# Kernel tuning notes

Hardware: AMD Instinct MI355X
Metric: run time of the kernel (lower is better)

The kernel has to match this reference:

```python
import jax, jax.numpy as jnp
import numpy as np

NUM_HEADS = 16


def setup_inputs() -> dict:
    key = jax.random.key(0)
    k1, k2, k3 = jax.random.split(key, 3)
    x = jax.random.normal(k1, (2, 2048, 1024), dtype=jnp.float32)
    w_qkv = jax.random.normal(k2, (3072, 1024), dtype=jnp.float32) * 0.02
    b_qkv = jax.random.normal(k3, (3072,), dtype=jnp.float32) * 0.02
    return {"x": x, "w_qkv": w_qkv, "b_qkv": b_qkv}


def reference(x, w_qkv, b_qkv):
    b, s, _ = x.shape
    d_model = w_qkv.shape[0] // 3
    head_dim = d_model // NUM_HEADS
    # fused QKV projection (torch Linear: x @ W^T + b)
    qkv = x @ w_qkv.T + b_qkv                      # [b, s, 3*d_model]
    qkv = qkv.reshape(b, s, NUM_HEADS, 3 * head_dim)
    qkv = jnp.transpose(qkv, (0, 2, 1, 3))          # [b, h, s, 3*hd]
    q, k, v = jnp.split(qkv, 3, axis=-1)            # each [b, h, s, hd]
    scale = 1.0 / np.sqrt(head_dim).astype(np.float32)
    scores = jnp.einsum("bhqd,bhkd->bhqk", q, k) * scale
    attn = jax.nn.softmax(scores, axis=-1)
    values = jnp.einsum("bhqk,bhkd->bhqd", attn, v)  # [b, h, s, hd]
    # Faithful to source: reshape WITHOUT permuting heads back (head-interleaved)
    return values.reshape(b, s, d_model)
```

## Files before the change

kernel.cpp:

```cpp
#include <hip/hip_runtime.h>
#include <cstdint>

typedef unsigned short ushort_t;

#define M_ROWS 4096
#define N_COLS 3072
#define K_DIM  1024
#define S_LEN  2048
#define NHEADS 16
#define HDIM   64
#define QSCALE 0.1803368801111204f

typedef __bf16 bf16_t;
typedef bf16_t  bf16x8  __attribute__((ext_vector_type(8)));
typedef short   shortx4 __attribute__((ext_vector_type(4)));
typedef float   floatx4 __attribute__((ext_vector_type(4)));
typedef ushort_t ushortx4 __attribute__((ext_vector_type(4)));

union U32x2S4 { unsigned u[2]; shortx4 s; };

__device__ __forceinline__ unsigned short f2bf(float f) {
  unsigned u = __float_as_uint(f);
  u += 0x7FFFu + ((u >> 16) & 1u);
  return (unsigned short)(u >> 16);
}

__device__ __forceinline__ unsigned pkbf(float a, float b) {
  unsigned ua = __float_as_uint(a) + 0x8000u;
  unsigned ub = __float_as_uint(b) + 0x8000u;
  return __builtin_amdgcn_perm(ub, ua, 0x07060302u);
}

__device__ __forceinline__ unsigned cvtpk(float a, float b) {
#if __has_builtin(__builtin_amdgcn_cvt_pk_bf16_f32)
  auto t = __builtin_amdgcn_cvt_pk_bf16_f32(a, b);
  unsigned r;
  __builtin_memcpy(&r, &t, 4);
  return r;
#else
  return pkbf(a, b);
#endif
}

__device__ __forceinline__ float fexp2(float x) {
#if __has_builtin(__builtin_amdgcn_exp2f)
  return __builtin_amdgcn_exp2f(x);
#else
  float r; asm volatile("v_exp_f32 %0, %1\n\ts_nop 1" : "=v"(r) : "v"(x)); return r;
#endif
}

__device__ __forceinline__ void gload_lds16(const void* g, void* l) {
  __builtin_amdgcn_global_load_lds(
      (const __attribute__((address_space(1))) unsigned int*)g,
      (__attribute__((address_space(3))) unsigned int*)l,
      16, 0, 0);
}

__global__ __launch_bounds__(256) void cvt_bf16_kernel(
    const float* __restrict__ x, const float* __restrict__ w,
    ushort_t* __restrict__ Xb, ushort_t* __restrict__ Wb) {
  const int NX8 = (M_ROWS * K_DIM) / 8;
  int i = blockIdx.x * 256 + threadIdx.x;
  const float4* src;
  ushort_t* dst;
  int idx;
  if (i < NX8) { src = (const float4*)x; dst = Xb; idx = i; }
  else         { src = (const float4*)w; dst = Wb; idx = i - NX8; }
  float4 a = src[2 * idx];
  float4 b = src[2 * idx + 1];
  uint4 o;
  o.x = cvtpk(a.x, a.y);
  o.y = cvtpk(a.z, a.w);
  o.z = cvtpk(b.x, b.y);
  o.w = cvtpk(b.z, b.w);
  *(uint4*)(dst + 8 * (size_t)idx) = o;
}

__global__ __launch_bounds__(256) void qkv_gemm_kernel(
    const ushort_t* __restrict__ Xb, const ushort_t* __restrict__ Wb,
    const float* __restrict__ bias,
    ushort_t* __restrict__ Qb, ushort_t* __restrict__ Kb, ushort_t* __restrict__ Vb) {
  __shared__ ushort_t As[128 * 64];
  __shared__ ushort_t Bs[128 * 64];
  const int tid = threadIdx.x;
  const int l = tid & 63, w = tid >> 6;
  const int quad = l >> 4, lj = l & 15;
  const int m0 = blockIdx.y * 128, n0 = blockIdx.x * 128;
  const int wm = (w & 1) * 64, wn = (w >> 1) * 64;

  floatx4 acc[4][4] = {};

  const int srow = w * 32 + (l >> 3);
  const int scol = ((l & 7) ^ (l >> 3)) * 8;
  const ushort_t* gA = Xb + (size_t)(m0 + srow) * K_DIM + scol;
  const ushort_t* gB = Wb + (size_t)(n0 + srow) * K_DIM + scol;
  ushort_t* lA = As + (w * 32) * 64;
  ushort_t* lB = Bs + (w * 32) * 64;

  const int swr = lj & 7;

  for (int k0 = 0; k0 < K_DIM; k0 += 64) {
    __syncthreads();
#pragma unroll
    for (int c = 0; c < 4; ++c) {
      gload_lds16(gA + (size_t)(c * 8) * K_DIM + k0, lA + c * 8 * 64);
      gload_lds16(gB + (size_t)(c * 8) * K_DIM + k0, lB + c * 8 * 64);
    }
    __syncthreads();
#pragma unroll
    for (int kk = 0; kk < 2; ++kk) {
      const int ch = ((kk * 4 + quad) ^ swr) * 8;
      bf16x8 aF[4], bF[4];
#pragma unroll
      for (int i = 0; i < 4; ++i)
        aF[i] = *(const bf16x8*)(As + (wm + i * 16 + lj) * 64 + ch);
#pragma unroll
      for (int j = 0; j < 4; ++j)
        bF[j] = *(const bf16x8*)(Bs + (wn + j * 16 + lj) * 64 + ch);
#pragma unroll
      for (int i = 0; i < 4; ++i)
#pragma unroll
        for (int j = 0; j < 4; ++j)
          acc[i][j] = __builtin_amdgcn_mfma_f32_16x16x32_bf16(aF[i], bF[j], acc[i][j], 0, 0, 0);
    }
  }

#pragma unroll
  for (int j = 0; j < 4; ++j) {
    const int n = n0 + wn + j * 16 + lj;
    const int h = n / 192;
    const int r = n - h * 192;
    const int seg = r >> 6;
    const int d = r & 63;
    const float bv = bias[n];
    ushort_t* dst = (seg == 0) ? Qb : (seg == 1) ? Kb : Vb;
    const float scl = (seg == 0) ? QSCALE : 1.0f;
    const size_t base = (size_t)h * S_LEN * HDIM + d;
#pragma unroll
    for (int i = 0; i < 4; ++i) {
#pragma unroll
      for (int rg = 0; rg < 4; ++rg) {
        const int m = m0 + wm + i * 16 + quad * 4 + rg;
        const int bi = m >> 11;
        const int si = m & 2047;
        dst[base + ((size_t)bi * NHEADS * S_LEN + si) * HDIM] =
            f2bf((acc[i][j][rg] + bv) * scl);
      }
    }
  }
}

__global__ __launch_bounds__(512, 2) void attn_kernel(
    const ushort_t* __restrict__ Qb, const ushort_t* __restrict__ Kb,
    const ushort_t* __restrict__ Vb, float* __restrict__ out) {
  __shared__ ushort_t Ks[2][128 * 64];
  __shared__ ushort_t Vs[2][64 * 140];
  const int tid = threadIdx.x;
  const int l = tid & 63, w = tid >> 6;
  const int quad = l >> 4, lj = l & 15;
  const int id = (blockIdx.x & 7) * 32 + (blockIdx.x >> 3);
  const int bh = id >> 3;
  const int qt = id & 7;
  const int q0 = qt * 256 + w * 32;
  const size_t headoff = (size_t)bh * S_LEN * HDIM;

  bf16x8 qF[2][2];
#pragma unroll
  for (int qh = 0; qh < 2; ++qh)
#pragma unroll
    for (int kk = 0; kk < 2; ++kk)
      qF[qh][kk] = *(const bf16x8*)(Qb + headoff +
                                    (size_t)(q0 + qh * 16 + lj) * HDIM +
                                    kk * 32 + quad * 8);

  floatx4 accO[2][4] = {};
  float l_runA[2] = {0.f, 0.f}, l_runB[2] = {0.f, 0.f};

  const int kr = tid >> 3;
  const int kc = ((tid & 7) ^ (kr & 7)) * 8;
  const ushort_t* gK = Kb + headoff + (size_t)kr * HDIM + kc;

  const int dq = tid & 15;
  const int spw = tid >> 4;
  const ushort_t* gV = Vb + headoff + dq * 4;
  const int swz = (dq >> 2) << 1;

  const int swk = lj & 7;

  {
    uint2 va[2], vb[2];
#pragma unroll
    for (int R = 0; R < 2; ++R) {
      const ushort_t* g = gV + (size_t)(2 * (R * 32 + spw)) * HDIM;
      va[R] = *(const uint2*)g;
      vb[R] = *(const uint2*)(g + HDIM);
    }
#pragma unroll
    for (int c = 0; c < 2; ++c)
      gload_lds16(gK + (size_t)(c * 64) * HDIM, &Ks[0][0] + tid * 8 + c * 64 * 64);
    unsigned* vdst = (unsigned*)&Vs[0][0];
#pragma unroll
    for (int R = 0; R < 2; ++R) {
      const int sp = R * 32 + spw;
      unsigned o0 = __builtin_amdgcn_perm(vb[R].x, va[R].x, 0x05040100u);
      unsigned o1 = __builtin_amdgcn_perm(vb[R].x, va[R].x, 0x07060302u);
      unsigned o2 = __builtin_amdgcn_perm(vb[R].y, va[R].y, 0x05040100u);
      unsigned o3 = __builtin_amdgcn_perm(vb[R].y, va[R].y, 0x07060302u);
      const int sp2 = sp ^ swz;
      vdst[(4 * dq + 0) * 70 + sp2] = o0;
      vdst[(4 * dq + 1) * 70 + sp2] = o1;
      vdst[(4 * dq + 2) * 70 + sp2] = o2;
      vdst[(4 * dq + 3) * 70 + sp2] = o3;
    }
  }
  __syncthreads();

  for (int kb = 0; kb < 16; ++kb) {
    const int cur = kb & 1;
    const ushort_t* Kc = &Ks[cur][0];
    const ushort_t* Vc = &Vs[cur][0];

    uint2 va[2], vb[2];
    if (kb < 15) {
      const int kv1 = (kb + 1) * 128;
#pragma unroll
      for (int R = 0; R < 2; ++R) {
        const ushort_t* g = gV + (size_t)(kv1 + 2 * (R * 32 + spw)) * HDIM;
        va[R] = *(const uint2*)g;
        vb[R] = *(const uint2*)(g + HDIM);
      }
#pragma unroll
      for (int c = 0; c < 2; ++c)
        gload_lds16(gK + (size_t)(kv1 + c * 64) * HDIM,
                    &Ks[cur ^ 1][0] + tid * 8 + c * 64 * 64);
    }

    floatx4 accST[2][8];
#pragma unroll
    for (int c = 0; c < 8; ++c) {
      const ushort_t* krow = Kc + (c * 16 + lj) * 64;
      bf16x8 kF0 = *(const bf16x8*)(krow + ((quad ^ swk) * 8));
      bf16x8 kF1 = *(const bf16x8*)(krow + (((quad ^ swk) ^ 4) * 8));
#pragma unroll
      for (int qh = 0; qh < 2; ++qh) {
        floatx4 z = {0.f, 0.f, 0.f, 0.f};
        z = __builtin_amdgcn_mfma_f32_16x16x32_bf16(kF0, qF[qh][0], z, 0, 0, 0);
        accST[qh][c] =
            __builtin_amdgcn_mfma_f32_16x16x32_bf16(kF1, qF[qh][1], z, 0, 0, 0);
      }
    }

    shortx4 aP[2][8];
#pragma unroll
    for (int qh = 0; qh < 2; ++qh) {
      float lsA = 0.f, lsB = 0.f;
#pragma unroll
      for (int c = 0; c < 8; ++c) {
        float p0 = fexp2(accST[qh][c][0]);
        float p1 = fexp2(accST[qh][c][1]);
        float p2 = fexp2(accST[qh][c][2]);
        float p3 = fexp2(accST[qh][c][3]);
        lsA += p0 + p1;
        lsB += p2 + p3;
        U32x2S4 t;
        t.u[0] = cvtpk(p0, p1);
        t.u[1] = cvtpk(p2, p3);
        aP[qh][c] = t.s;
      }
      l_runA[qh] += lsA;
      l_runB[qh] += lsB;
    }

    if (kb < 15) {
      unsigned* vdst = (unsigned*)&Vs[cur ^ 1][0];
#pragma unroll
      for (int R = 0; R < 2; ++R) {
        const int sp = R * 32 + spw;
        unsigned o0 = __builtin_amdgcn_perm(vb[R].x, va[R].x, 0x05040100u);
        unsigned o1 = __builtin_amdgcn_perm(vb[R].x, va[R].x, 0x07060302u);
        unsigned o2 = __builtin_amdgcn_perm(vb[R].y, va[R].y, 0x05040100u);
        unsigned o3 = __builtin_amdgcn_perm(vb[R].y, va[R].y, 0x07060302u);
        const int sp2 = sp ^ swz;
        vdst[(4 * dq + 0) * 70 + sp2] = o0;
        vdst[(4 * dq + 1) * 70 + sp2] = o1;
        vdst[(4 * dq + 2) * 70 + sp2] = o2;
        vdst[(4 * dq + 3) * 70 + sp2] = o3;
      }
    }

#pragma unroll
    for (int dt = 0; dt < 4; ++dt) {
      const ushort_t* vp = Vc + (dt * 16 + lj) * 140 + (quad ^ dt) * 4;
#pragma unroll
      for (int c = 0; c < 8; ++c) {
        shortx4 vF = *(const shortx4*)(vp + c * 16);
        accO[0][dt] =
            __builtin_amdgcn_mfma_f32_16x16x16bf16_1k(aP[0][c], vF, accO[0][dt], 0, 0, 0);
        accO[1][dt] =
            __builtin_amdgcn_mfma_f32_16x16x16bf16_1k(aP[1][c], vF, accO[1][dt], 0, 0, 0);
      }
    }

    __syncthreads();
  }

#pragma unroll
  for (int qh = 0; qh < 2; ++qh) {
    float ls = l_runA[qh] + l_runB[qh];
    ls += __shfl_xor(ls, 16, 64);
    ls += __shfl_xor(ls, 32, 64);
    const float inv = 1.0f / ls;
    const int sbase = (l & 48) | (quad * 4);
    float iv[4];
    iv[0] = __shfl(inv, sbase + 0, 64);
    iv[1] = __shfl(inv, sbase + 1, 64);
    iv[2] = __shfl(inv, sbase + 2, 64);
    iv[3] = __shfl(inv, sbase + 3, 64);
#pragma unroll
    for (int dt = 0; dt < 4; ++dt) {
#pragma unroll
      for (int rg = 0; rg < 4; ++rg) {
        const int q = q0 + qh * 16 + quad * 4 + rg;
        out[headoff + (size_t)q * HDIM + dt * 16 + lj] = accO[qh][dt][rg] * iv[rg];
      }
    }
  }
}

extern "C" void kernel_launch(void* const* d_in, const int* in_sizes, int n_in,
                              void* d_out, int out_size, void* d_ws, size_t ws_size,
                              hipStream_t stream) {
  (void)in_sizes; (void)n_in; (void)out_size; (void)ws_size;
  const float* x  = (const float*)d_in[0];
  const float* wq = (const float*)d_in[1];
  const float* bq = (const float*)d_in[2];
  float* out = (float*)d_out;

  char* ws = (char*)d_ws;
  ushort_t* Qb = (ushort_t*)(ws);
  ushort_t* Kb = (ushort_t*)(ws + 8388608);
  ushort_t* Vb = (ushort_t*)(ws + 16777216);
  ushort_t* Xb = (ushort_t*)(ws + 25165824);
  ushort_t* Wb = (ushort_t*)(ws + 33554432);

  cvt_bf16_kernel<<<3584, 256, 0, stream>>>(x, wq, Xb, Wb);
  qkv_gemm_kernel<<<dim3(N_COLS / 128, M_ROWS / 128), 256, 0, stream>>>(Xb, Wb, bq, Qb, Kb, Vb);
  attn_kernel<<<256, 512, 0, stream>>>(Qb, Kb, Vb, out);
}
```

Before: 160.4 us.

## Split attention KV range across two wave halves and merge in LDS

Each attention block now covers 128 queries instead of 256. The 8 waves split into two halves, each handling half of the key/value sequence (tiles 0-7 and 8-15), and the partial outputs and row sums are combined through shared memory at the end. The grid doubles to 512 blocks and the launch bounds ask for 4 blocks per SM, which raises parallelism and occupancy on the attention stage. In exchange, the previous double-buffered prefetch overlap is lost: loads now happen synchronously between two barriers each iteration. The final merge step also adds LDS traffic and register pressure.

```diff
diff --git a/kernel.cpp b/kernel.cpp
--- a/kernel.cpp
+++ b/kernel.cpp
@@ -151,7 +151,7 @@
   }
 }
 
-__global__ __launch_bounds__(512, 2) void attn_kernel(
+__global__ __launch_bounds__(512, 4) void attn_kernel(
     const ushort_t* __restrict__ Qb, const ushort_t* __restrict__ Kb,
     const ushort_t* __restrict__ Vb, float* __restrict__ out) {
   __shared__ ushort_t Ks[2][128 * 64];
@@ -159,10 +159,12 @@
   const int tid = threadIdx.x;
   const int l = tid & 63, w = tid >> 6;
   const int quad = l >> 4, lj = l & 15;
-  const int id = (blockIdx.x & 7) * 32 + (blockIdx.x >> 3);
-  const int bh = id >> 3;
-  const int qt = id & 7;
-  const int q0 = qt * 256 + w * 32;
+  const int half = w >> 2;
+  const int qg = w & 3;
+  const int id = (blockIdx.x & 7) * 64 + (blockIdx.x >> 3);
+  const int bh = id >> 4;
+  const int qt = id & 15;
+  const int q0 = qt * 128 + qg * 32;
   const size_t headoff = (size_t)bh * S_LEN * HDIM;
 
   bf16x8 qF[2][2];
@@ -175,7 +177,7 @@
                                     kk * 32 + quad * 8);
 
   floatx4 accO[2][4] = {};
-  float l_runA[2] = {0.f, 0.f}, l_runB[2] = {0.f, 0.f};
+  float l_run[2] = {0.f, 0.f};
 
   const int kr = tid >> 3;
   const int kc = ((tid & 7) ^ (kr & 7)) * 8;
@@ -188,54 +190,39 @@
 
   const int swk = lj & 7;
 
-  {
-    uint2 va[2], vb[2];
-#pragma unroll
-    for (int R = 0; R < 2; ++R) {
-      const ushort_t* g = gV + (size_t)(2 * (R * 32 + spw)) * HDIM;
-      va[R] = *(const uint2*)g;
-      vb[R] = *(const uint2*)(g + HDIM);
-    }
+  auto STAGE = [&](int s, int tile) {
+    const int kv = tile * 128;
 #pragma unroll
     for (int c = 0; c < 2; ++c)
-      gload_lds16(gK + (size_t)(c * 64) * HDIM, &Ks[0][0] + tid * 8 + c * 64 * 64);
-    unsigned* vdst = (unsigned*)&Vs[0][0];
+      gload_lds16(gK + (size_t)(kv + c * 64) * HDIM,
+                  &Ks[s][0] + tid * 8 + c * 64 * 64);
+    unsigned* vdst = (unsigned*)&Vs[s][0];
 #pragma unroll
     for (int R = 0; R < 2; ++R) {
       const int sp = R * 32 + spw;
-      unsigned o0 = __builtin_amdgcn_perm(vb[R].x, va[R].x, 0x05040100u);
-      unsigned o1 = __builtin_amdgcn_perm(vb[R].x, va[R].x, 0x07060302u);
-      unsigned o2 = __builtin_amdgcn_perm(vb[R].y, va[R].y, 0x05040100u);
-      unsigned o3 = __builtin_amdgcn_perm(vb[R].y, va[R].y, 0x07060302u);
+      const ushort_t* g = gV + (size_t)(kv + 2 * sp) * HDIM;
+      const uint2 v0 = *(const uint2*)g;
+      const uint2 v1 = *(const uint2*)(g + HDIM);
+      unsigned o0 = __builtin_amdgcn_perm(v1.x, v0.x, 0x05040100u);
+      unsigned o1 = __builtin_amdgcn_perm(v1.x, v0.x, 0x07060302u);
+      unsigned o2 = __builtin_amdgcn_perm(v1.y, v0.y, 0x05040100u);
+      unsigned o3 = __builtin_amdgcn_perm(v1.y, v0.y, 0x07060302u);
       const int sp2 = sp ^ swz;
       vdst[(4 * dq + 0) * 70 + sp2] = o0;
       vdst[(4 * dq + 1) * 70 + sp2] = o1;
       vdst[(4 * dq + 2) * 70 + sp2] = o2;
       vdst[(4 * dq + 3) * 70 + sp2] = o3;
     }
-  }
+  };
+
+  STAGE(0, 0);
+  STAGE(1, 8);
   __syncthreads();
 
-  for (int kb = 0; kb < 16; ++kb) {
-    const int cur = kb & 1;
-    const ushort_t* Kc = &Ks[cur][0];
-    const ushort_t* Vc = &Vs[cur][0];
-
-    uint2 va[2], vb[2];
-    if (kb < 15) {
-      const int kv1 = (kb + 1) * 128;
-#pragma unroll
-      for (int R = 0; R < 2; ++R) {
-        const ushort_t* g = gV + (size_t)(kv1 + 2 * (R * 32 + spw)) * HDIM;
-        va[R] = *(const uint2*)g;
-        vb[R] = *(const uint2*)(g + HDIM);
-      }
-#pragma unroll
-      for (int c = 0; c < 2; ++c)
-        gload_lds16(gK + (size_t)(kv1 + c * 64) * HDIM,
-                    &Ks[cur ^ 1][0] + tid * 8 + c * 64 * 64);
-    }
-
+  const ushort_t* Kc = &Ks[half][0];
+  const ushort_t* Vc = &Vs[half][0];
+
+  for (int r = 0; r < 8; ++r) {
     floatx4 accST[2][8];
 #pragma unroll
     for (int c = 0; c < 8; ++c) {
@@ -268,25 +255,7 @@
         t.u[1] = cvtpk(p2, p3);
         aP[qh][c] = t.s;
       }
-      l_runA[qh] += lsA;
-      l_runB[qh] += lsB;
-    }
-
-    if (kb < 15) {
-      unsigned* vdst = (unsigned*)&Vs[cur ^ 1][0];
-#pragma unroll
-      for (int R = 0; R < 2; ++R) {
-        const int sp = R * 32 + spw;
-        unsigned o0 = __builtin_amdgcn_perm(vb[R].x, va[R].x, 0x05040100u);
-        unsigned o1 = __builtin_amdgcn_perm(vb[R].x, va[R].x, 0x07060302u);
-        unsigned o2 = __builtin_amdgcn_perm(vb[R].y, va[R].y, 0x05040100u);
-        unsigned o3 = __builtin_amdgcn_perm(vb[R].y, va[R].y, 0x07060302u);
-        const int sp2 = sp ^ swz;
-        vdst[(4 * dq + 0) * 70 + sp2] = o0;
-        vdst[(4 * dq + 1) * 70 + sp2] = o1;
-        vdst[(4 * dq + 2) * 70 + sp2] = o2;
-        vdst[(4 * dq + 3) * 70 + sp2] = o3;
-      }
+      l_run[qh] += lsA + lsB;
     }
 
 #pragma unroll
@@ -303,26 +272,49 @@
     }
 
     __syncthreads();
-  }
-
-#pragma unroll
-  for (int qh = 0; qh < 2; ++qh) {
-    float ls = l_runA[qh] + l_runB[qh];
-    ls += __shfl_xor(ls, 16, 64);
-    ls += __shfl_xor(ls, 32, 64);
-    const float inv = 1.0f / ls;
-    const int sbase = (l & 48) | (quad * 4);
-    float iv[4];
-    iv[0] = __shfl(inv, sbase + 0, 64);
-    iv[1] = __shfl(inv, sbase + 1, 64);
-    iv[2] = __shfl(inv, sbase + 2, 64);
-    iv[3] = __shfl(inv, sbase + 3, 64);
-#pragma unroll
-    for (int dt = 0; dt < 4; ++dt) {
-#pragma unroll
-      for (int rg = 0; rg < 4; ++rg) {
-        const int q = q0 + qh * 16 + quad * 4 + rg;
-        out[headoff + (size_t)q * HDIM + dt * 16 + lj] = accO[qh][dt][rg] * iv[rg];
+    if (r < 7) {
+      STAGE(0, r + 1);
+      STAGE(1, r + 9);
+    }
+    __syncthreads();
+  }
+
+  float* mrg = (float*)&Ks[0][0];
+  float* lbf = (float*)&Vs[0][0];
+  if (half == 1) {
+#pragma unroll
+    for (int qh = 0; qh < 2; ++qh) {
+#pragma unroll
+      for (int dt = 0; dt < 4; ++dt)
+#pragma unroll
+        for (int rg = 0; rg < 4; ++rg)
+          mrg[((qg * 2 + qh) * 16 + dt * 4 + rg) * 64 + l] = accO[qh][dt][rg];
+      lbf[(qg * 2 + qh) * 64 + l] = l_run[qh];
+    }
+  }
+  __syncthreads();
+  if (half == 0) {
+#pragma unroll
+    for (int qh = 0; qh < 2; ++qh) {
+      float ls = l_run[qh] + lbf[(qg * 2 + qh) * 64 + l];
+      ls += __shfl_xor(ls, 16, 64);
+      ls += __shfl_xor(ls, 32, 64);
+      const float inv = 1.0f / ls;
+      const int sbase = (l & 48) | (quad * 4);
+      float iv[4];
+      iv[0] = __shfl(inv, sbase + 0, 64);
+      iv[1] = __shfl(inv, sbase + 1, 64);
+      iv[2] = __shfl(inv, sbase + 2, 64);
+      iv[3] = __shfl(inv, sbase + 3, 64);
+#pragma unroll
+      for (int dt = 0; dt < 4; ++dt) {
+#pragma unroll
+        for (int rg = 0; rg < 4; ++rg) {
+          const int q = q0 + qh * 16 + quad * 4 + rg;
+          const float o =
+              accO[qh][dt][rg] + mrg[((qg * 2 + qh) * 16 + dt * 4 + rg) * 64 + l];
+          out[headoff + (size_t)q * HDIM + dt * 16 + lj] = o * iv[rg];
+        }
       }
     }
   }
@@ -346,5 +338,5 @@
 
   cvt_bf16_kernel<<<3584, 256, 0, stream>>>(x, wq, Xb, Wb);
   qkv_gemm_kernel<<<dim3(N_COLS / 128, M_ROWS / 128), 256, 0, stream>>>(Xb, Wb, bq, Qb, Kb, Vb);
-  attn_kernel<<<256, 512, 0, stream>>>(Qb, Kb, Vb, out);
-}
+  attn_kernel<<<512, 512, 0, stream>>>(Qb, Kb, Vb, out);
+}
```

Result: slower. 221.4 us (+38.0%).
